# Kernel tuning notes

Hardware: AMD Instinct MI355X
Metric: run time of the kernel (lower is better)

## Reference

```python
import math
import jax, jax.numpy as jnp
import numpy as np

B, S, H, NH = 2, 1536, 2048, 16
DH = H // NH  # 128
FP16_MIN = float(jnp.finfo(jnp.float16).min)


def setup_inputs() -> dict:
    key = jax.random.key(0)
    ks = jax.random.split(key, 6)
    std = 0.02
    return {
        "x": jax.random.normal(ks[0], (B, S, H), dtype=jnp.float32),
        "attention_bias": jax.random.normal(ks[1], (B, NH, S, S), dtype=jnp.float32),
        "Wq": jax.random.normal(ks[2], (H, H), dtype=jnp.float32) * std,
        "Wk": jax.random.normal(ks[3], (H, H), dtype=jnp.float32) * std,
        "Wv": jax.random.normal(ks[4], (H, H), dtype=jnp.float32) * std,
        "Wo": jax.random.normal(ks[5], (H, H), dtype=jnp.float32) * std,
    }


def reference(x, attention_bias, Wq, Wk, Wv, Wo):
    b, s, h = x.shape
    # QKV projections (nn.Linear with bias=False: y = x @ W.T)
    q = (x @ Wq.T).reshape(b, s, NH, DH).transpose(0, 2, 1, 3)  # b h s d
    k = (x @ Wk.T).reshape(b, s, NH, DH).transpose(0, 2, 1, 3)
    v = (x @ Wv.T).reshape(b, s, NH, DH).transpose(0, 2, 1, 3)
    # bias[:, :, -s:, -s:] is identity here since bias is already [b,h,s,s]
    bias = attention_bias[:, :, -s:, -s:]
    # mask where tril(bias) == 0 (upper triangle and any exact zeros in lower)
    masked = jnp.tril(bias) == 0
    bias = jnp.where(masked, FP16_MIN, bias)
    # torch SDPA default scale = 1/sqrt(head_dim) (module's softmax_scale unused)
    scale = 1.0 / math.sqrt(DH)
    scores = jnp.einsum("bhqd,bhkd->bhqk", q, k) * scale + bias
    attn = jax.nn.softmax(scores, axis=-1)
    out = jnp.einsum("bhqk,bhkd->bhqd", attn, v)  # b h s d
    out = out.transpose(0, 2, 1, 3).reshape(b, s, h)  # b s (h d)
    return out @ Wo.T
```

## Files before the change

kernel.cpp:

```cpp
#include <hip/hip_runtime.h>
#include <cstdint>
#include <stddef.h>

typedef short short8 __attribute__((ext_vector_type(8)));
typedef float floatx4 __attribute__((ext_vector_type(4)));
typedef unsigned short ushortx4 __attribute__((ext_vector_type(4)));

#define MFMA16(a, b, c) __builtin_amdgcn_mfma_f32_16x16x32_bf16((a), (b), (c), 0, 0, 0)

static constexpr int Bv = 2, Sv = 1536, Hv = 2048, NHv = 16, DHv = 128;
static constexpr int Mv = Bv * Sv;
static constexpr float SCALE = 0.08838834764831845f;

__device__ inline unsigned short f2bf(float f) {
  union { float f; unsigned u; } c; c.f = f;
  unsigned u = c.u;
  u += 0x7fffu + ((u >> 16) & 1u);
  return (unsigned short)(u >> 16);
}

__device__ inline void async_copy16(const void* g, void* l) {
  auto gp = reinterpret_cast<__attribute__((address_space(1))) uint32_t*>(
      reinterpret_cast<uintptr_t>(g));
  auto lp = reinterpret_cast<__attribute__((address_space(3))) uint32_t*>(
      reinterpret_cast<uintptr_t>(l));
  __builtin_amdgcn_global_load_lds(gp, lp, 16, 0, 0);
}

__global__ void cvt_all_kernel(const float* __restrict__ x,
    const float* __restrict__ Wq, const float* __restrict__ Wk,
    const float* __restrict__ Wv, const float* __restrict__ Wo,
    unsigned short* __restrict__ xb, unsigned short* __restrict__ wqb,
    unsigned short* __restrict__ wkb, unsigned short* __restrict__ wvb,
    unsigned short* __restrict__ wob) {
  const int i = blockIdx.x * 256 + threadIdx.x;
  const int nx4 = (Mv * Hv) / 4;
  const float* src; unsigned short* dst; int j; float scl = 1.0f;
  if (i < nx4) {
    src = x; dst = xb; j = i;
  } else {
    const int i2 = i - nx4;
    const int wsel = i2 >> 20;
    j = i2 & ((1 << 20) - 1);
    if (wsel == 0)      { src = Wq; dst = wqb; scl = SCALE; }
    else if (wsel == 1) { src = Wk; dst = wkb; }
    else if (wsel == 2) { src = Wv; dst = wvb; }
    else                { src = Wo; dst = wob; }
  }
  const float4 v = reinterpret_cast<const float4*>(src)[j];
  ushortx4 o;
  o[0] = f2bf(v.x * scl); o[1] = f2bf(v.y * scl);
  o[2] = f2bf(v.z * scl); o[3] = f2bf(v.w * scl);
  reinterpret_cast<ushortx4*>(dst)[j] = o;
}

template <int TM, bool WF32>
__global__ __launch_bounds__(256) void gemm_bt_kernel(
    const unsigned short* __restrict__ A,
    const unsigned short* __restrict__ W0, const unsigned short* __restrict__ W1,
    const unsigned short* __restrict__ W2,
    void* __restrict__ C0, void* __restrict__ C1, void* __restrict__ C2) {
  constexpr int MI = TM / 32;
  __shared__ __align__(16) unsigned short As[2][TM * 64];
  __shared__ __align__(16) unsigned short Bs[2][128 * 64];
  const int z = blockIdx.z;
  const unsigned short* W = (z == 0) ? W0 : ((z == 1) ? W1 : W2);
  const int tid = threadIdx.x;
  const int w = tid >> 6, lane = tid & 63;
  const int quad = lane >> 4, l15 = lane & 15;
  const int wr = w >> 1, wc = w & 1;
  const int tileM = blockIdx.y * TM, tileN = blockIdx.x * 128;

  floatx4 acc[MI][4];
#pragma unroll
  for (int i = 0; i < MI; ++i)
#pragma unroll
    for (int j = 0; j < 4; ++j)
#pragma unroll
      for (int r = 0; r < 4; ++r) acc[i][j][r] = 0.0f;

  size_t aoff[MI]; int alb[MI];
#pragma unroll
  for (int m = 0; m < MI; ++m) {
    const int slot = m * 256 + tid;
    const int row = slot >> 3, blk = slot & 7;
    aoff[m] = (size_t)(tileM + row) * 2048 + ((blk ^ (row & 7)) * 8);
    alb[m] = (m * 256 + w * 64) * 8;
  }
  size_t boff[4]; int blb[4];
#pragma unroll
  for (int m = 0; m < 4; ++m) {
    const int slot = m * 256 + tid;
    const int row = slot >> 3, blk = slot & 7;
    boff[m] = (size_t)(tileN + row) * 2048 + ((blk ^ (row & 7)) * 8);
    blb[m] = (m * 256 + w * 64) * 8;
  }

#pragma unroll
  for (int m = 0; m < MI; ++m) async_copy16(A + aoff[m], As[0] + alb[m]);
#pragma unroll
  for (int m = 0; m < 4; ++m) async_copy16(W + boff[m], Bs[0] + blb[m]);
  __syncthreads();

  for (int t = 0; t < 32; ++t) {
    const int cur = t & 1;
    if (t < 31) {
      const int kn = (t + 1) * 64;
#pragma unroll
      for (int m = 0; m < MI; ++m)
        async_copy16(A + aoff[m] + kn, As[cur ^ 1] + alb[m]);
#pragma unroll
      for (int m = 0; m < 4; ++m)
        async_copy16(W + boff[m] + kn, Bs[cur ^ 1] + blb[m]);
    }
    const unsigned short* as_ = As[cur];
    const unsigned short* bs_ = Bs[cur];
#pragma unroll
    for (int kk = 0; kk < 2; ++kk) {
      const int swz = (((kk * 4 + quad) ^ (l15 & 7)) * 8);
      short8 af[MI], bfr[4];
#pragma unroll
      for (int i = 0; i < MI; ++i)
        af[i] = *(const short8*)(as_ + (wr * (TM / 2) + i * 16 + l15) * 64 + swz);
#pragma unroll
      for (int j = 0; j < 4; ++j)
        bfr[j] = *(const short8*)(bs_ + (wc * 64 + j * 16 + l15) * 64 + swz);
#pragma unroll
      for (int i = 0; i < MI; ++i)
#pragma unroll
        for (int j = 0; j < 4; ++j) acc[i][j] = MFMA16(af[i], bfr[j], acc[i][j]);
    }
    __syncthreads();
  }

  void* C = (z == 0) ? C0 : ((z == 1) ? C1 : C2);
#pragma unroll
  for (int i = 0; i < MI; ++i) {
#pragma unroll
    for (int r = 0; r < 4; ++r) {
      const int row = tileM + wr * (TM / 2) + i * 16 + quad * 4 + r;
#pragma unroll
      for (int j = 0; j < 4; ++j) {
        const int col = tileN + wc * 64 + j * 16 + l15;
        if (WF32)
          ((float*)C)[(size_t)row * 2048 + col] = acc[i][j][r];
        else
          ((unsigned short*)C)[(size_t)row * 2048 + col] = f2bf(acc[i][j][r]);
      }
    }
  }
}

__global__ __launch_bounds__(256) void vtrans_kernel(
    const unsigned short* __restrict__ V, unsigned short* __restrict__ Vtg) {
  __shared__ unsigned short Vs[64 * 132];
  const int t0 = blockIdx.x * 64, h = blockIdx.y, b = blockIdx.z;
  const int tid = threadIdx.x;
  const int w = tid >> 6, lane = tid & 63;
#pragma unroll
  for (int m = 0; m < 4; ++m) {
    const int idx = m * 256 + tid;
    const int tr = idx >> 4, blk = idx & 15;
    const unsigned short* src = V + ((size_t)(b * Sv) + t0 + tr) * Hv + h * DHv + blk * 8;
    ushortx4 v0 = *(const ushortx4*)(src);
    ushortx4 v1 = *(const ushortx4*)(src + 4);
    *(ushortx4*)(Vs + tr * 132 + blk * 8) = v0;
    *(ushortx4*)(Vs + tr * 132 + blk * 8 + 4) = v1;
  }
  __syncthreads();
  const size_t obase = ((size_t)(b * NHv + h) * DHv) * Sv + t0;
#pragma unroll 4
  for (int p = 0; p < 32; ++p) {
    const int d = p * 4 + w;
    Vtg[obase + (size_t)d * Sv + lane] = Vs[lane * 132 + d];
  }
}

__global__ __launch_bounds__(256) void attn_kernel(
    const unsigned short* __restrict__ Qg, const unsigned short* __restrict__ Kg,
    const unsigned short* __restrict__ Vtg, const float* __restrict__ bias,
    unsigned short* __restrict__ Og) {
  __shared__ __align__(16) unsigned short Ks[2][64 * 128];
  __shared__ __align__(16) unsigned short Vt[2][128 * 64];
  __shared__ __align__(16) unsigned short Ps[4 * 16 * 64];

  const int xb = blockIdx.x;
  const int qt = (xb & 1) ? (23 - (xb >> 1)) : (xb >> 1);
  const int h = blockIdx.y, b = blockIdx.z;
  const int q0 = qt * 64;
  const int tid = threadIdx.x;
  const int w = tid >> 6, lane = tid & 63;
  const int quad = lane >> 4, l15 = lane & 15;

  const size_t bh_base = (size_t)(b * Sv) * Hv + (size_t)h * DHv;
  const size_t vt_base = ((size_t)(b * NHv + h) * DHv) * Sv;

  short8 qf[4];
  {
    const unsigned short* qbase = Qg + bh_base + (size_t)(q0 + w * 16 + l15) * Hv;
#pragma unroll
    for (int kk = 0; kk < 4; ++kk)
      qf[kk] = *(const short8*)(qbase + kk * 32 + quad * 8);
  }

  floatx4 o[8];
#pragma unroll
  for (int n = 0; n < 8; ++n)
#pragma unroll
    for (int r = 0; r < 4; ++r) o[n][r] = 0.0f;
  float lrow[4] = {0.0f, 0.0f, 0.0f, 0.0f};

  const float* biasbase = bias + (size_t)(b * NHv + h) * Sv * Sv;
  unsigned short* pw = Ps + w * 1024;

  size_t koff[4], voff[4]; int lbs[4];
#pragma unroll
  for (int m = 0; m < 4; ++m) {
    const int sK = m * 256 + tid;
    const int rK = sK >> 4, bK = sK & 15;
    koff[m] = bh_base + (size_t)rK * Hv + ((bK ^ (rK & 15)) * 8);
    const int sV = m * 256 + tid;
    const int rV = sV >> 3, bV = sV & 7;
    voff[m] = vt_base + (size_t)rV * Sv + ((bV ^ (rV & 7)) * 8);
    lbs[m] = (m * 256 + w * 64) * 8;
  }

  float bv[4][4];
#pragma unroll
  for (int r = 0; r < 4; ++r) {
    const size_t brow = (size_t)(q0 + w * 16 + quad * 4 + r) * Sv;
#pragma unroll
    for (int j = 0; j < 4; ++j) bv[r][j] = biasbase[brow + j * 16 + l15];
  }

#pragma unroll
  for (int m = 0; m < 4; ++m) {
    async_copy16(Kg + koff[m], Ks[0] + lbs[m]);
    async_copy16(Vtg + voff[m], Vt[0] + lbs[m]);
  }
  __syncthreads();

  for (int kt = 0; kt <= qt; ++kt) {
    const int k0 = kt * 64;
    const int cur = kt & 1;

    if (kt < qt) {
      const int k1 = k0 + 64;
#pragma unroll
      for (int m = 0; m < 4; ++m) {
        async_copy16(Kg + koff[m] + (size_t)k1 * Hv, Ks[cur ^ 1] + lbs[m]);
        async_copy16(Vtg + voff[m] + k1, Vt[cur ^ 1] + lbs[m]);
      }
    }

    const int kn = (kt < qt) ? k0 + 64 : k0;
    float bvn[4][4];
#pragma unroll
    for (int r = 0; r < 4; ++r) {
      const size_t brow = (size_t)(q0 + w * 16 + quad * 4 + r) * Sv;
#pragma unroll
      for (int j = 0; j < 4; ++j) bvn[r][j] = biasbase[brow + kn + j * 16 + l15];
    }

    const unsigned short* ks_ = Ks[cur];
    const unsigned short* vt_ = Vt[cur];
    floatx4 sacc[4];
#pragma unroll
    for (int j = 0; j < 4; ++j) {
#pragma unroll
      for (int r = 0; r < 4; ++r) sacc[j][r] = 0.0f;
      const int kr = j * 16 + l15;
#pragma unroll
      for (int kk = 0; kk < 4; ++kk) {
        const int g = kk * 4 + quad;
        short8 bfrag = *(const short8*)(ks_ + kr * 128 + (g ^ (kr & 15)) * 8);
        sacc[j] = MFMA16(qf[kk], bfrag, sacc[j]);
      }
    }

    const bool diag = (kt == qt);
#pragma unroll
    for (int r = 0; r < 4; ++r) {
      const int qrow = q0 + w * 16 + quad * 4 + r;
      const int prow = quad * 4 + r;
      float acc_l = 0.0f;
#pragma unroll
      for (int j = 0; j < 4; ++j) {
        const int col = j * 16 + l15;
        float p = __expf(sacc[j][r] + bv[r][j]);
        if (diag && (k0 + col) > qrow) p = 0.0f;
        acc_l += p;
        pw[prow * 64 + ((col >> 3) ^ (prow & 7)) * 8 + (col & 7)] = f2bf(p);
      }
      lrow[r] += acc_l;
    }
#pragma unroll
    for (int r = 0; r < 4; ++r)
#pragma unroll
      for (int j = 0; j < 4; ++j) bv[r][j] = bvn[r][j];

#pragma unroll
    for (int kk = 0; kk < 2; ++kk) {
      const int g = kk * 4 + quad;
      short8 pa = *(const short8*)(pw + l15 * 64 + (g ^ (l15 & 7)) * 8);
#pragma unroll
      for (int n = 0; n < 8; ++n) {
        const int dr = n * 16 + l15;
        short8 vbf = *(const short8*)(vt_ + dr * 64 + (g ^ (dr & 7)) * 8);
        o[n] = MFMA16(pa, vbf, o[n]);
      }
    }

    __syncthreads();
  }

#pragma unroll
  for (int r = 0; r < 4; ++r) {
    float ls = lrow[r];
#pragma unroll
    for (int off = 1; off < 16; off <<= 1) ls += __shfl_xor(ls, off, 64);
    const float inv = 1.0f / ls;
    const int qrow = q0 + w * 16 + quad * 4 + r;
    const size_t rowbase = bh_base + (size_t)qrow * Hv;
#pragma unroll
    for (int n = 0; n < 8; ++n)
      Og[rowbase + n * 16 + l15] = f2bf(o[n][r] * inv);
  }
}

extern "C" void kernel_launch(void* const* d_in, const int* in_sizes, int n_in,
                              void* d_out, int out_size, void* d_ws, size_t ws_size,
                              hipStream_t stream) {
  const float* x = (const float*)d_in[0];
  const float* bias = (const float*)d_in[1];
  const float* Wq = (const float*)d_in[2];
  const float* Wk = (const float*)d_in[3];
  const float* Wv = (const float*)d_in[4];
  const float* Wo = (const float*)d_in[5];
  float* out = (float*)d_out;

  unsigned short* xb = (unsigned short*)d_ws;
  unsigned short* wqb = xb + (size_t)Mv * Hv;
  unsigned short* wkb = wqb + (size_t)Hv * Hv;
  unsigned short* wvb = wkb + (size_t)Hv * Hv;
  unsigned short* wob = wvb + (size_t)Hv * Hv;
  unsigned short* qb = wob + (size_t)Hv * Hv;
  unsigned short* kb = qb + (size_t)Mv * Hv;
  unsigned short* vb = kb + (size_t)Mv * Hv;
  unsigned short* ob = vb + (size_t)Mv * Hv;
  unsigned short* vtb = xb;
  const size_t needed = ((size_t)Mv * Hv * 5 + (size_t)Hv * Hv * 4) * 2;
  if (ws_size < needed) return;

  const int cvt_n = (Mv * Hv) / 4 + Hv * Hv;
  cvt_all_kernel<<<dim3(cvt_n / 256), 256, 0, stream>>>(
      x, Wq, Wk, Wv, Wo, xb, wqb, wkb, wvb, wob);

  gemm_bt_kernel<128, false><<<dim3(16, 24, 3), 256, 0, stream>>>(
      xb, wqb, wkb, wvb, qb, kb, vb);

  vtrans_kernel<<<dim3(24, 16, 2), 256, 0, stream>>>(vb, vtb);

  attn_kernel<<<dim3(24, NHv, Bv), 256, 0, stream>>>(qb, kb, vtb, bias, ob);

  gemm_bt_kernel<64, true><<<dim3(16, 48, 1), 256, 0, stream>>>(
      ob, wob, wob, wob, out, out, out);
}
```

Baseline: 617.9 us.

## Fuse QKV projections into one kernel sharing A tiles, add MFMA priority hints

Replaces the three-way gridded QKV GEMM with a single kernel that loads each activation tile once and multiplies it against Wq, Wk and Wv tiles, keeping three accumulator sets per thread. It also raises wave priority around the MFMA sections of the attention kernel, and switches the output projection to 128-row tiles. The aim is to cut redundant activation loads and launch count. In exchange the fused kernel drops double buffering, needs far more registers, and both GEMMs launch fewer blocks, which may reduce occupancy and latency hiding.

```diff
diff --git a/kernel.cpp b/kernel.cpp
--- a/kernel.cpp
+++ b/kernel.cpp
@@ -54,17 +54,115 @@
   reinterpret_cast<ushortx4*>(dst)[j] = o;
 }
 
+__global__ __launch_bounds__(256, 2) void qkv_fused_kernel(
+    const unsigned short* __restrict__ A,
+    const unsigned short* __restrict__ Wq, const unsigned short* __restrict__ Wk,
+    const unsigned short* __restrict__ Wv,
+    unsigned short* __restrict__ Cq, unsigned short* __restrict__ Ck,
+    unsigned short* __restrict__ Cv) {
+  __shared__ __align__(16) unsigned short As[128 * 64];
+  __shared__ __align__(16) unsigned short Bs[3][128 * 64];
+  const int tid = threadIdx.x;
+  const int w = tid >> 6, lane = tid & 63;
+  const int quad = lane >> 4, l15 = lane & 15;
+  const int wr = w >> 1, wc = w & 1;
+  const int tileM = blockIdx.y * 128, tileN = blockIdx.x * 128;
+
+  floatx4 aq[4][4], ak[4][4], av[4][4];
+#pragma unroll
+  for (int i = 0; i < 4; ++i)
+#pragma unroll
+    for (int j = 0; j < 4; ++j)
+#pragma unroll
+      for (int r = 0; r < 4; ++r) { aq[i][j][r] = 0.0f; ak[i][j][r] = 0.0f; av[i][j][r] = 0.0f; }
+
+  size_t aoff[4], boff[4]; int lbs[4];
+#pragma unroll
+  for (int m = 0; m < 4; ++m) {
+    const int slot = m * 256 + tid;
+    const int row = slot >> 3, blk = slot & 7;
+    const int sw = (blk ^ (row & 7)) * 8;
+    aoff[m] = (size_t)(tileM + row) * 2048 + sw;
+    boff[m] = (size_t)(tileN + row) * 2048 + sw;
+    lbs[m] = (m * 256 + w * 64) * 8;
+  }
+
+  for (int k0 = 0; k0 < 2048; k0 += 64) {
+    __syncthreads();
+#pragma unroll
+    for (int m = 0; m < 4; ++m) async_copy16(A + aoff[m] + k0, As + lbs[m]);
+#pragma unroll
+    for (int m = 0; m < 4; ++m) async_copy16(Wq + boff[m] + k0, Bs[0] + lbs[m]);
+#pragma unroll
+    for (int m = 0; m < 4; ++m) async_copy16(Wk + boff[m] + k0, Bs[1] + lbs[m]);
+#pragma unroll
+    for (int m = 0; m < 4; ++m) async_copy16(Wv + boff[m] + k0, Bs[2] + lbs[m]);
+    __syncthreads();
+#pragma unroll
+    for (int kk = 0; kk < 2; ++kk) {
+      const int swz = (((kk * 4 + quad) ^ (l15 & 7)) * 8);
+      short8 af[4];
+#pragma unroll
+      for (int i = 0; i < 4; ++i)
+        af[i] = *(const short8*)(As + (wr * 64 + i * 16 + l15) * 64 + swz);
+      {
+        short8 bq[4];
+#pragma unroll
+        for (int j = 0; j < 4; ++j)
+          bq[j] = *(const short8*)(Bs[0] + (wc * 64 + j * 16 + l15) * 64 + swz);
+#pragma unroll
+        for (int i = 0; i < 4; ++i)
+#pragma unroll
+          for (int j = 0; j < 4; ++j) aq[i][j] = MFMA16(af[i], bq[j], aq[i][j]);
+      }
+      {
+        short8 bk[4];
+#pragma unroll
+        for (int j = 0; j < 4; ++j)
+          bk[j] = *(const short8*)(Bs[1] + (wc * 64 + j * 16 + l15) * 64 + swz);
+#pragma unroll
+        for (int i = 0; i < 4; ++i)
+#pragma unroll
+          for (int j = 0; j < 4; ++j) ak[i][j] = MFMA16(af[i], bk[j], ak[i][j]);
+      }
+      {
+        short8 bv[4];
+#pragma unroll
+        for (int j = 0; j < 4; ++j)
+          bv[j] = *(const short8*)(Bs[2] + (wc * 64 + j * 16 + l15) * 64 + swz);
+#pragma unroll
+        for (int i = 0; i < 4; ++i)
+#pragma unroll
+          for (int j = 0; j < 4; ++j) av[i][j] = MFMA16(af[i], bv[j], av[i][j]);
+      }
+    }
+  }
+
+#pragma unroll
+  for (int i = 0; i < 4; ++i) {
+#pragma unroll
+    for (int r = 0; r < 4; ++r) {
+      const size_t row = tileM + wr * 64 + i * 16 + quad * 4 + r;
+#pragma unroll
+      for (int j = 0; j < 4; ++j) {
+        const int col = tileN + wc * 64 + j * 16 + l15;
+        Cq[row * 2048 + col] = f2bf(aq[i][j][r]);
+        Ck[row * 2048 + col] = f2bf(ak[i][j][r]);
+        Cv[row * 2048 + col] = f2bf(av[i][j][r]);
+      }
+    }
+  }
+}
+
 template <int TM, bool WF32>
 __global__ __launch_bounds__(256) void gemm_bt_kernel(
     const unsigned short* __restrict__ A,
-    const unsigned short* __restrict__ W0, const unsigned short* __restrict__ W1,
-    const unsigned short* __restrict__ W2,
-    void* __restrict__ C0, void* __restrict__ C1, void* __restrict__ C2) {
+    const unsigned short* __restrict__ W0,
+    void* __restrict__ C0) {
   constexpr int MI = TM / 32;
   __shared__ __align__(16) unsigned short As[2][TM * 64];
   __shared__ __align__(16) unsigned short Bs[2][128 * 64];
-  const int z = blockIdx.z;
-  const unsigned short* W = (z == 0) ? W0 : ((z == 1) ? W1 : W2);
+  const unsigned short* W = W0;
   const int tid = threadIdx.x;
   const int w = tid >> 6, lane = tid & 63;
   const int quad = lane >> 4, l15 = lane & 15;
@@ -133,7 +231,7 @@
     __syncthreads();
   }
 
-  void* C = (z == 0) ? C0 : ((z == 1) ? C1 : C2);
+  void* C = C0;
 #pragma unroll
   for (int i = 0; i < MI; ++i) {
 #pragma unroll
@@ -265,6 +363,7 @@
     const unsigned short* ks_ = Ks[cur];
     const unsigned short* vt_ = Vt[cur];
     floatx4 sacc[4];
+    __builtin_amdgcn_s_setprio(1);
 #pragma unroll
     for (int j = 0; j < 4; ++j) {
 #pragma unroll
@@ -277,6 +376,7 @@
         sacc[j] = MFMA16(qf[kk], bfrag, sacc[j]);
       }
     }
+    __builtin_amdgcn_s_setprio(0);
 
     const bool diag = (kt == qt);
 #pragma unroll
@@ -299,6 +399,7 @@
 #pragma unroll
       for (int j = 0; j < 4; ++j) bv[r][j] = bvn[r][j];
 
+    __builtin_amdgcn_s_setprio(1);
 #pragma unroll
     for (int kk = 0; kk < 2; ++kk) {
       const int g = kk * 4 + quad;
@@ -310,6 +411,7 @@
         o[n] = MFMA16(pa, vbf, o[n]);
       }
     }
+    __builtin_amdgcn_s_setprio(0);
 
     __syncthreads();
   }
@@ -356,13 +458,12 @@
   cvt_all_kernel<<<dim3(cvt_n / 256), 256, 0, stream>>>(
       x, Wq, Wk, Wv, Wo, xb, wqb, wkb, wvb, wob);
 
-  gemm_bt_kernel<128, false><<<dim3(16, 24, 3), 256, 0, stream>>>(
+  qkv_fused_kernel<<<dim3(16, 24), 256, 0, stream>>>(
       xb, wqb, wkb, wvb, qb, kb, vb);
 
   vtrans_kernel<<<dim3(24, 16, 2), 256, 0, stream>>>(vb, vtb);
 
   attn_kernel<<<dim3(24, NHv, Bv), 256, 0, stream>>>(qb, kb, vtb, bias, ob);
 
-  gemm_bt_kernel<64, true><<<dim3(16, 48, 1), 256, 0, stream>>>(
-      ob, wob, wob, wob, out, out, out);
-}
+  gemm_bt_kernel<128, true><<<dim3(16, 24), 256, 0, stream>>>(ob, wob, out);
+}
```

Result: no change. 613.2 us (-0.8%).
